# Optimization experiments

Measured on AMD Instinct MI355X. Metric: run time of the kernel, lower is better.

## Reference

```python
import math
import jax, jax.numpy as jnp
import numpy as np

E = 64   # embed_size (also per-head dim)
H = 8    # heads
B = 4
T = 2048


def setup_inputs() -> dict:
    key = jax.random.key(0)
    ks = jax.random.split(key, 8)
    s_in = 1.0 / math.sqrt(E)
    s_out = 1.0 / math.sqrt(H * E)
    return {
        "values": jax.random.normal(ks[0], (B, T, E), dtype=jnp.float32),
        "keys": jax.random.normal(ks[1], (B, T, E), dtype=jnp.float32),
        "queries": jax.random.normal(ks[2], (B, T, E), dtype=jnp.float32),
        # Linear(E, E*H, bias=False) weights, stored as [in, out] for x @ W
        "Wv": jax.random.uniform(ks[3], (E, E * H), jnp.float32, -s_in, s_in),
        "Wk": jax.random.uniform(ks[4], (E, E * H), jnp.float32, -s_in, s_in),
        "Wq": jax.random.uniform(ks[5], (E, E * H), jnp.float32, -s_in, s_in),
        # unifyheads: Linear(H*E, E)
        "Wu": jax.random.uniform(ks[6], (H * E, E), jnp.float32, -s_out, s_out),
        "bu": jax.random.uniform(ks[7], (E,), jnp.float32, -s_out, s_out),
    }


def reference(values, keys, queries, Wv, Wk, Wq, Wu, bu):
    b, t, e = keys.shape
    h = H
    v = (values @ Wv).reshape(b, t, h, e)   # bthe
    k = (keys @ Wk).reshape(b, t, h, e)
    q = (queries @ Wq).reshape(b, t, h, e)
    dot = jnp.einsum('bthe,bihe->bhti', q, k) / math.sqrt(e)  # [b,h,t,i]
    # NOTE: source applies softmax over dim=2 (the query axis t), faithfully kept
    attention = jax.nn.softmax(dot, axis=2)
    out = jnp.einsum('bhtd,bdhe->bthe', attention, v).reshape(b, t, h * e)
    return out @ Wu + bu
```

## Files before the change

### kernel.cpp

```cpp
#include <hip/hip_runtime.h>


typedef __attribute__((ext_vector_type(8))) __bf16 bf16x8;
typedef __attribute__((ext_vector_type(8))) unsigned short ushort8;
typedef __attribute__((ext_vector_type(4))) unsigned short ushort4v;
typedef __attribute__((ext_vector_type(4))) short short4v;
typedef __attribute__((ext_vector_type(4))) float f32x4;
typedef unsigned int uint32;

constexpr int B_ = 4;
constexpr int T_ = 2048;
constexpr int H_ = 8;
constexpr int E_ = 64;
constexpr int BH_ = B_ * H_;
constexpr int SZ_ = 8;
constexpr int NP_ = 2;
constexpr float QSCALE_ = 0.125f * 1.4426950408889634f;

__device__ inline uint32 f2bf1(float f) {
  uint32 u = __builtin_bit_cast(uint32, f);
  return (u + 0x7fffu + ((u >> 16) & 1u)) >> 16;
}
__device__ inline uint32 pk2(float a, float b) {
#if __has_builtin(__builtin_amdgcn_cvt_pk_bf16_f32)
  return __builtin_bit_cast(uint32, __builtin_amdgcn_cvt_pk_bf16_f32(a, b));
#else
  return f2bf1(a) | (f2bf1(b) << 16);
#endif
}
__device__ inline float bf2f(uint32 bits) {
  return __builtin_bit_cast(float, bits << 16);
}
__device__ inline bf16x8 ld8(const unsigned short* p) {
  return __builtin_bit_cast(bf16x8, *(const ushort8*)p);
}
__device__ inline short4v ld4(const unsigned short* p) {
  return __builtin_bit_cast(short4v, *(const ushort4v*)p);
}
#define MFMA16(a, b, c) __builtin_amdgcn_mfma_f32_16x16x32_bf16(a, b, c, 0, 0, 0)
#define EXP2(x) __builtin_amdgcn_exp2f(x)

__device__ inline f32x4 pv_mfma(short4v a, short4v b, f32x4 c) {
#if __has_builtin(__builtin_amdgcn_mfma_f32_16x16x16bf16_1k)
  return __builtin_amdgcn_mfma_f32_16x16x16bf16_1k(a, b, c, 0, 0, 0);
#else
  asm("v_mfma_f32_16x16x16_bf16 %0, %1, %2, %0" : "+v"(c) : "v"(a), "v"(b));
  return c;
#endif
}

__device__ inline void dma16(const unsigned short* g, unsigned short* l) {
  __builtin_amdgcn_global_load_lds(
      (const __attribute__((address_space(1))) void*)g,
      (__attribute__((address_space(3))) void*)l, 16, 0, 0);
}

__global__ __launch_bounds__(512) void proj_kernel(
    const float* __restrict__ Xq, const float* __restrict__ Xk,
    const float* __restrict__ Xv, const float* __restrict__ Wq,
    const float* __restrict__ Wk, const float* __restrict__ Wv,
    unsigned short* __restrict__ Yq, unsigned short* __restrict__ Yk,
    unsigned short* __restrict__ Yv) {
  constexpr int RT = 8;
  __shared__ float xs[RT][E_];
  const int z = blockIdx.y;
  const float* X = (z == 0) ? Xq : (z == 1) ? Xk : Xv;
  const float* W = (z == 0) ? Wq : (z == 1) ? Wk : Wv;
  unsigned short* Y = (z == 0) ? Yq : (z == 1) ? Yk : Yv;
  const float scale = (z == 0) ? QSCALE_ : 1.0f;
  const int row0 = blockIdx.x * RT;
  const int tid = threadIdx.x;
  {
    const int r = tid >> 6, c = tid & 63;
    xs[r][c] = X[(row0 + r) * E_ + c];
  }
  __syncthreads();
  const int j = tid;
  const int h = j >> 6, e = j & 63;
  float acc[RT];
#pragma unroll
  for (int r = 0; r < RT; ++r) acc[r] = 0.f;
  for (int c = 0; c < E_; ++c) {
    const float w = W[c * (H_ * E_) + j];
#pragma unroll
    for (int r = 0; r < RT; ++r) acc[r] += xs[r][c] * w;
  }
#pragma unroll
  for (int r = 0; r < RT; ++r) {
    const int row = row0 + r;
    const int b = row >> 11, t = row & (T_ - 1);
    Y[(((size_t)(b * H_ + h) * T_ + t) << 6) + e] =
        (unsigned short)f2bf1(acc[r] * scale);
  }
}

__global__ __launch_bounds__(256, 4) void stats_kernel(
    const unsigned short* __restrict__ K16, const unsigned short* __restrict__ Q16,
    float* __restrict__ s_part) {
  const int g = blockIdx.x;
  const int x = g & 7, s = g >> 3;
  const int bh = x + 8 * (s >> 6);
  const int rem = s & 63;
  const int zi = rem >> 3;
  const int dblk = rem & 7;
  const int tid = threadIdx.x;
  const int w = tid >> 6, lane = tid & 63;
  const int lm = lane & 15, lq = lane >> 4;
  const int d0 = dblk * 256 + w * 64;
  const int tz0 = zi * (T_ / SZ_);
  const unsigned short* Kp = K16 + (size_t)bh * T_ * E_;
  const unsigned short* Qp = Q16 + (size_t)bh * T_ * E_;

  bf16x8 kf[4][2];
#pragma unroll
  for (int dt = 0; dt < 4; ++dt) {
    kf[dt][0] = ld8(&Kp[(size_t)(d0 + dt * 16 + lm) * E_ + lq * 8]);
    kf[dt][1] = ld8(&Kp[(size_t)(d0 + dt * 16 + lm) * E_ + 32 + lq * 8]);
  }
  f32x4 sacc[4];
#pragma unroll
  for (int dt = 0; dt < 4; ++dt) sacc[dt] = (f32x4){0.f, 0.f, 0.f, 0.f};
  const f32x4 zero = {0.f, 0.f, 0.f, 0.f};

  for (int t0 = tz0; t0 < tz0 + 256; t0 += 16) {
    const bf16x8 ql = ld8(&Qp[(size_t)(t0 + lm) * E_ + lq * 8]);
    const bf16x8 qh = ld8(&Qp[(size_t)(t0 + lm) * E_ + 32 + lq * 8]);
#pragma unroll
    for (int dt = 0; dt < 4; ++dt) {
      f32x4 c = MFMA16(kf[dt][0], ql, zero);
      c = MFMA16(kf[dt][1], qh, c);
#pragma unroll
      for (int r = 0; r < 4; ++r) sacc[dt][r] += EXP2(c[r]);
    }
  }
#pragma unroll
  for (int m = 1; m < 16; m <<= 1) {
#pragma unroll
    for (int dt = 0; dt < 4; ++dt)
#pragma unroll
      for (int r = 0; r < 4; ++r)
        sacc[dt][r] += __shfl_xor(sacc[dt][r], m);
  }
  if (lm == 0) {
#pragma unroll
    for (int dt = 0; dt < 4; ++dt)
#pragma unroll
      for (int r = 0; r < 4; ++r)
        s_part[((size_t)zi * BH_ + bh) * T_ + d0 + dt * 16 + lq * 4 + r] =
            sacc[dt][r];
  }
}

__global__ __launch_bounds__(256) void scale_kernel(
    const unsigned short* __restrict__ V16, const float* __restrict__ s_part,
    unsigned short* __restrict__ Vt16) {
  __shared__ float ts[64][68];
  __shared__ float sinv_s[64];
  const int bh = blockIdx.y;
  const int d0 = blockIdx.x * 64;
  const unsigned short* Vp = V16 + (size_t)bh * T_ * E_;
  const int tid = threadIdx.x;
  if (tid < 64) {
    float s = 0.f;
#pragma unroll
    for (int z = 0; z < SZ_; ++z)
      s += s_part[((size_t)z * BH_ + bh) * T_ + d0 + tid];
    sinv_s[tid] = 1.0f / s;
  }
  __syncthreads();
  for (int idx = tid; idx < 64 * 8; idx += 256) {
    const int r = idx >> 3, c8 = idx & 7;
    const ushort8 v8 = *(const ushort8*)&Vp[(size_t)(d0 + r) * E_ + c8 * 8];
    const float is = sinv_s[r];
#pragma unroll
    for (int k = 0; k < 8; ++k) ts[r][c8 * 8 + k] = bf2f(v8[k]) * is;
  }
  __syncthreads();
  for (int idx = tid; idx < 64 * 16; idx += 256) {
    const int e = idx >> 4, d4 = idx & 15;
    uint2 o;
    o.x = pk2(ts[d4 * 4 + 0][e], ts[d4 * 4 + 1][e]);
    o.y = pk2(ts[d4 * 4 + 2][e], ts[d4 * 4 + 3][e]);
    *(uint2*)&Vt16[((size_t)bh * E_ + e) * T_ + d0 + d4 * 4] = o;
  }
}

__global__ __launch_bounds__(256, 4) void apply_kernel(
    const unsigned short* __restrict__ K16, const unsigned short* __restrict__ Q16,
    const unsigned short* __restrict__ Vt16, float* __restrict__ o_part) {
  __shared__ __align__(16) unsigned short K_s[2][32 * 64];
  __shared__ __align__(16) unsigned short V_s[2][64 * 32];
  const int g = blockIdx.x;
  const int xcd = g & 7, slot = g >> 3;
  const int bh = xcd + 8 * (slot >> 5);
  const int rem = slot & 31;
  const int np = rem >> 4;
  const int tblk = rem & 15;
  const int b = bh >> 3, h = bh & 7;
  const int tid = threadIdx.x;
  const int w = tid >> 6, lane = tid & 63;
  const int lm = lane & 15, lq = lane >> 4;
  const int t0 = tblk * 128 + w * 32;
  const int dbase = np * (T_ / NP_);
  constexpr int NC = (T_ / NP_) / 32;
  const unsigned short* Kp = K16 + (size_t)bh * T_ * E_;
  const unsigned short* Qp = Q16 + (size_t)bh * T_ * E_;
  const unsigned short* Vp = Vt16 + (size_t)bh * E_ * T_;

  const int kr = lane >> 3, kp = lane & 7, ks = kp ^ kr;
  const unsigned short* gK = Kp + (size_t)(w * 8 + kr) * E_ + ks * 8;
  const int ve = w * 16 + (lane >> 2), vseg = lane & 3;
  const unsigned short* gV = Vp + (size_t)ve * T_ + vseg * 8;
  unsigned short* lK0 = &K_s[0][w * 512];
  unsigned short* lK1 = &K_s[1][w * 512];
  unsigned short* lV0 = &V_s[0][w * 512];
  unsigned short* lV1 = &V_s[1][w * 512];

  bf16x8 qf[2][2];
#pragma unroll
  for (int tt = 0; tt < 2; ++tt) {
    qf[tt][0] = ld8(&Qp[(size_t)(t0 + tt * 16 + lm) * E_ + lq * 8]);
    qf[tt][1] = ld8(&Qp[(size_t)(t0 + tt * 16 + lm) * E_ + 32 + lq * 8]);
  }
  f32x4 acc[2][4];
#pragma unroll
  for (int tt = 0; tt < 2; ++tt)
#pragma unroll
    for (int ec = 0; ec < 4; ++ec) acc[tt][ec] = (f32x4){0.f, 0.f, 0.f, 0.f};
  const f32x4 zero = {0.f, 0.f, 0.f, 0.f};

  dma16(gK + (size_t)dbase * E_, lK0);
  dma16(gV + dbase, lV0);
  __syncthreads();

  for (int c = 0; c < NC; ++c) {
    const int cur = c & 1;
    if (c + 1 < NC) {
      const int dn = dbase + (c + 1) * 32;
      dma16(gK + (size_t)dn * E_, cur ? lK0 : lK1);
      dma16(gV + dn, cur ? lV0 : lV1);
    }
    const unsigned short* Kb = K_s[cur];
    const unsigned short* Vb = V_s[cur];
    bf16x8 kf[2][2];
#pragma unroll
    for (int half = 0; half < 2; ++half)
#pragma unroll
      for (int hi = 0; hi < 2; ++hi)
        kf[half][hi] =
            ld8(&Kb[(half * 16 + lm) * 64 + (((hi * 4 + lq) ^ (lm & 7)) * 8)]);
    short4v vf[4][2];
#pragma unroll
    for (int ec = 0; ec < 4; ++ec)
#pragma unroll
      for (int half = 0; half < 2; ++half)
        vf[ec][half] = ld4(&Vb[(ec * 16 + lm) * 32 + half * 16 + lq * 4]);

#pragma unroll
    for (int tt = 0; tt < 2; ++tt) {
      f32x4 c0 = MFMA16(kf[0][0], qf[tt][0], zero);
      c0 = MFMA16(kf[0][1], qf[tt][1], c0);
      f32x4 c1 = MFMA16(kf[1][0], qf[tt][0], zero);
      c1 = MFMA16(kf[1][1], qf[tt][1], c1);
      const uint32 b00 = pk2(EXP2(c0[0]), EXP2(c0[1]));
      const uint32 b01 = pk2(EXP2(c0[2]), EXP2(c0[3]));
      const uint32 b10 = pk2(EXP2(c1[0]), EXP2(c1[1]));
      const uint32 b11 = pk2(EXP2(c1[2]), EXP2(c1[3]));
      const short4v eB0 = __builtin_bit_cast(short4v, make_uint2(b00, b01));
      const short4v eB1 = __builtin_bit_cast(short4v, make_uint2(b10, b11));
#pragma unroll
      for (int ec = 0; ec < 4; ++ec) {
        acc[tt][ec] = pv_mfma(vf[ec][0], eB0, acc[tt][ec]);
        acc[tt][ec] = pv_mfma(vf[ec][1], eB1, acc[tt][ec]);
      }
    }
    __syncthreads();
  }

  float* op_base = o_part + (size_t)np * BH_ * T_ * E_;
#pragma unroll
  for (int tt = 0; tt < 2; ++tt) {
    const int t = t0 + tt * 16 + lm;
#pragma unroll
    for (int ec = 0; ec < 4; ++ec) {
      float* op = &op_base[((size_t)(b * T_ + t) * H_ + h) * E_ + ec * 16 + lq * 4];
      *(float4*)op = make_float4(acc[tt][ec][0], acc[tt][ec][1],
                                 acc[tt][ec][2], acc[tt][ec][3]);
    }
  }
}

__global__ __launch_bounds__(256) void unify_kernel(
    const float* __restrict__ o0, const float* __restrict__ o1,
    const float* __restrict__ Wu, const float* __restrict__ bu,
    float* __restrict__ out) {
  constexpr int RT = 16;
  __shared__ float xs[RT][H_ * E_];
  const int row0 = blockIdx.x * RT;
  const int tid = threadIdx.x;
  for (int idx = tid; idx < RT * 128; idx += 256) {
    const int r = idx >> 7, c4 = idx & 127;
    const float4 a = *(const float4*)&o0[(size_t)(row0 + r) * 512 + c4 * 4];
    const float4 bv = *(const float4*)&o1[(size_t)(row0 + r) * 512 + c4 * 4];
    xs[r][c4 * 4 + 0] = a.x + bv.x;
    xs[r][c4 * 4 + 1] = a.y + bv.y;
    xs[r][c4 * 4 + 2] = a.z + bv.z;
    xs[r][c4 * 4 + 3] = a.w + bv.w;
  }
  __syncthreads();
  const int j = tid & 63;
  const int rg = tid >> 6;
  float acc[4] = {0.f, 0.f, 0.f, 0.f};
  for (int c = 0; c < 512; ++c) {
    const float w = Wu[c * 64 + j];
#pragma unroll
    for (int r = 0; r < 4; ++r) acc[r] += xs[rg * 4 + r][c] * w;
  }
  const float bias = bu[j];
#pragma unroll
  for (int r = 0; r < 4; ++r)
    out[(size_t)(row0 + rg * 4 + r) * 64 + j] = acc[r] + bias;
}

extern "C" void kernel_launch(void* const* d_in, const int* in_sizes, int n_in,
                              void* d_out, int out_size, void* d_ws, size_t ws_size,
                              hipStream_t stream) {
  const float* values  = (const float*)d_in[0];
  const float* keys    = (const float*)d_in[1];
  const float* queries = (const float*)d_in[2];
  const float* Wv      = (const float*)d_in[3];
  const float* Wk      = (const float*)d_in[4];
  const float* Wq      = (const float*)d_in[5];
  const float* Wu      = (const float*)d_in[6];
  const float* bu      = (const float*)d_in[7];
  float* out = (float*)d_out;

  const size_t NQ = (size_t)BH_ * T_ * E_;
  unsigned short* q_bf  = (unsigned short*)d_ws;
  unsigned short* k_bf  = q_bf + NQ;
  unsigned short* v_bf  = k_bf + NQ;
  unsigned short* vt_bf = v_bf + NQ;
  float* o_ws   = (float*)(vt_bf + NQ);
  float* s_part = o_ws + (size_t)NP_ * NQ;

  proj_kernel<<<dim3(B_ * T_ / 8, 3), 512, 0, stream>>>(
      queries, keys, values, Wq, Wk, Wv, q_bf, k_bf, v_bf);
  stats_kernel<<<T_ / 256 * BH_ * SZ_, 256, 0, stream>>>(k_bf, q_bf, s_part);
  scale_kernel<<<dim3(T_ / 64, BH_), 256, 0, stream>>>(v_bf, s_part, vt_bf);
  apply_kernel<<<BH_ * (T_ / 128) * NP_, 256, 0, stream>>>(k_bf, q_bf, vt_bf, o_ws);
  unify_kernel<<<B_ * T_ / 16, 256, 0, stream>>>(o_ws, o_ws + NQ, Wu, bu, out);
}
```

Before: 289.6 us.

## Enlarge apply chunks with permuted V layout, stage Q in LDS for stats

The apply kernel now loads 64-key chunks of K and V per iteration instead of 32. The scale kernel writes V-transposed in a permuted order, so each lane fetches one 8-wide vector and splits it into the two 4-wide MFMA operands, replacing two narrower LDS reads. The stats kernel stages Q tiles through double-buffered LDS using async global-to-LDS loads instead of direct global loads. The projection kernel handles 16 rows per block to reuse weight loads. The changes raise LDS use per block, which may reduce occupancy.

```diff
diff --git a/kernel.cpp b/kernel.cpp
--- a/kernel.cpp
+++ b/kernel.cpp
@@ -2,8 +2,8 @@
 
 
 typedef __attribute__((ext_vector_type(8))) __bf16 bf16x8;
+typedef __attribute__((ext_vector_type(8))) short short8v;
 typedef __attribute__((ext_vector_type(8))) unsigned short ushort8;
-typedef __attribute__((ext_vector_type(4))) unsigned short ushort4v;
 typedef __attribute__((ext_vector_type(4))) short short4v;
 typedef __attribute__((ext_vector_type(4))) float f32x4;
 typedef unsigned int uint32;
@@ -34,8 +34,13 @@
 __device__ inline bf16x8 ld8(const unsigned short* p) {
   return __builtin_bit_cast(bf16x8, *(const ushort8*)p);
 }
-__device__ inline short4v ld4(const unsigned short* p) {
-  return __builtin_bit_cast(short4v, *(const ushort4v*)p);
+__device__ inline short4v lo4(bf16x8 v) {
+  short8v s = __builtin_bit_cast(short8v, v);
+  return __builtin_shufflevector(s, s, 0, 1, 2, 3);
+}
+__device__ inline short4v hi4(bf16x8 v) {
+  short8v s = __builtin_bit_cast(short8v, v);
+  return __builtin_shufflevector(s, s, 4, 5, 6, 7);
 }
 #define MFMA16(a, b, c) __builtin_amdgcn_mfma_f32_16x16x32_bf16(a, b, c, 0, 0, 0)
 #define EXP2(x) __builtin_amdgcn_exp2f(x)
@@ -61,7 +66,7 @@
     const float* __restrict__ Wk, const float* __restrict__ Wv,
     unsigned short* __restrict__ Yq, unsigned short* __restrict__ Yk,
     unsigned short* __restrict__ Yv) {
-  constexpr int RT = 8;
+  constexpr int RT = 16;
   __shared__ float xs[RT][E_];
   const int z = blockIdx.y;
   const float* X = (z == 0) ? Xq : (z == 1) ? Xk : Xv;
@@ -70,10 +75,9 @@
   const float scale = (z == 0) ? QSCALE_ : 1.0f;
   const int row0 = blockIdx.x * RT;
   const int tid = threadIdx.x;
-  {
-    const int r = tid >> 6, c = tid & 63;
-    xs[r][c] = X[(row0 + r) * E_ + c];
-  }
+#pragma unroll
+  for (int idx = tid; idx < RT * E_; idx += 512)
+    xs[idx >> 6][idx & 63] = X[(size_t)(row0 + (idx >> 6)) * E_ + (idx & 63)];
   __syncthreads();
   const int j = tid;
   const int h = j >> 6, e = j & 63;
@@ -97,6 +101,7 @@
 __global__ __launch_bounds__(256, 4) void stats_kernel(
     const unsigned short* __restrict__ K16, const unsigned short* __restrict__ Q16,
     float* __restrict__ s_part) {
+  __shared__ __align__(16) unsigned short Q_s[2][64 * 64];
   const int g = blockIdx.x;
   const int x = g & 7, s = g >> 3;
   const int bh = x + 8 * (s >> 6);
@@ -111,6 +116,12 @@
   const unsigned short* Kp = K16 + (size_t)bh * T_ * E_;
   const unsigned short* Qp = Q16 + (size_t)bh * T_ * E_;
 
+  const int kr = lane >> 3, kp = lane & 7;
+  const unsigned short* gQ =
+      Qp + (size_t)(tz0 + w * 16 + kr) * E_ + (kp ^ kr) * 8;
+  unsigned short* lQ0 = &Q_s[0][w * 1024];
+  unsigned short* lQ1 = &Q_s[1][w * 1024];
+
   bf16x8 kf[4][2];
 #pragma unroll
   for (int dt = 0; dt < 4; ++dt) {
@@ -122,16 +133,35 @@
   for (int dt = 0; dt < 4; ++dt) sacc[dt] = (f32x4){0.f, 0.f, 0.f, 0.f};
   const f32x4 zero = {0.f, 0.f, 0.f, 0.f};
 
-  for (int t0 = tz0; t0 < tz0 + 256; t0 += 16) {
-    const bf16x8 ql = ld8(&Qp[(size_t)(t0 + lm) * E_ + lq * 8]);
-    const bf16x8 qh = ld8(&Qp[(size_t)(t0 + lm) * E_ + 32 + lq * 8]);
-#pragma unroll
-    for (int dt = 0; dt < 4; ++dt) {
-      f32x4 c = MFMA16(kf[dt][0], ql, zero);
-      c = MFMA16(kf[dt][1], qh, c);
-#pragma unroll
-      for (int r = 0; r < 4; ++r) sacc[dt][r] += EXP2(c[r]);
-    }
+  dma16(gQ, lQ0);
+  dma16(gQ + 8 * E_, lQ0 + 512);
+  __syncthreads();
+
+  for (int c = 0; c < 4; ++c) {
+    const unsigned short* Qb = Q_s[c & 1];
+    bf16x8 qf[4][2];
+#pragma unroll
+    for (int tt = 0; tt < 4; ++tt)
+#pragma unroll
+      for (int half = 0; half < 2; ++half)
+        qf[tt][half] =
+            ld8(&Qb[(tt * 16 + lm) * 64 + (((half * 4 + lq) ^ (lm & 7)) * 8)]);
+    if (c < 3) {
+      const unsigned short* gn = gQ + (size_t)(c + 1) * 64 * E_;
+      unsigned short* ln = (c & 1) ? lQ0 : lQ1;
+      dma16(gn, ln);
+      dma16(gn + 8 * E_, ln + 512);
+    }
+#pragma unroll
+    for (int tt = 0; tt < 4; ++tt)
+#pragma unroll
+      for (int dt = 0; dt < 4; ++dt) {
+        f32x4 cc = MFMA16(kf[dt][0], qf[tt][0], zero);
+        cc = MFMA16(kf[dt][1], qf[tt][1], cc);
+#pragma unroll
+        for (int r = 0; r < 4; ++r) sacc[dt][r] += EXP2(cc[r]);
+      }
+    __syncthreads();
   }
 #pragma unroll
   for (int m = 1; m < 16; m <<= 1) {
@@ -177,19 +207,26 @@
   }
   __syncthreads();
   for (int idx = tid; idx < 64 * 16; idx += 256) {
-    const int e = idx >> 4, d4 = idx & 15;
-    uint2 o;
-    o.x = pk2(ts[d4 * 4 + 0][e], ts[d4 * 4 + 1][e]);
-    o.y = pk2(ts[d4 * 4 + 2][e], ts[d4 * 4 + 3][e]);
-    *(uint2*)&Vt16[((size_t)bh * E_ + e) * T_ + d0 + d4 * 4] = o;
+    const int e = idx >> 4, q = idx & 15;
+    float v[4];
+#pragma unroll
+    for (int j = 0; j < 4; ++j) {
+      const int pos = q * 4 + j;
+      const int c32 = pos >> 5, i = pos & 31;
+      const int lqp = i >> 3, u = i & 7;
+      const int dl = (u < 4) ? (lqp * 4 + u) : (16 + lqp * 4 + (u - 4));
+      v[j] = ts[c32 * 32 + dl][e];
+    }
+    uint2 o = make_uint2(pk2(v[0], v[1]), pk2(v[2], v[3]));
+    *(uint2*)&Vt16[((size_t)bh * E_ + e) * T_ + d0 + q * 4] = o;
   }
 }
 
 __global__ __launch_bounds__(256, 4) void apply_kernel(
     const unsigned short* __restrict__ K16, const unsigned short* __restrict__ Q16,
     const unsigned short* __restrict__ Vt16, float* __restrict__ o_part) {
-  __shared__ __align__(16) unsigned short K_s[2][32 * 64];
-  __shared__ __align__(16) unsigned short V_s[2][64 * 32];
+  __shared__ __align__(16) unsigned short K_s[2][64 * 64];
+  __shared__ __align__(16) unsigned short V_s[2][64 * 64];
   const int g = blockIdx.x;
   const int xcd = g & 7, slot = g >> 3;
   const int bh = xcd + 8 * (slot >> 5);
@@ -202,19 +239,18 @@
   const int lm = lane & 15, lq = lane >> 4;
   const int t0 = tblk * 128 + w * 32;
   const int dbase = np * (T_ / NP_);
-  constexpr int NC = (T_ / NP_) / 32;
+  constexpr int NC = (T_ / NP_) / 64;
   const unsigned short* Kp = K16 + (size_t)bh * T_ * E_;
   const unsigned short* Qp = Q16 + (size_t)bh * T_ * E_;
   const unsigned short* Vp = Vt16 + (size_t)bh * E_ * T_;
 
-  const int kr = lane >> 3, kp = lane & 7, ks = kp ^ kr;
-  const unsigned short* gK = Kp + (size_t)(w * 8 + kr) * E_ + ks * 8;
-  const int ve = w * 16 + (lane >> 2), vseg = lane & 3;
-  const unsigned short* gV = Vp + (size_t)ve * T_ + vseg * 8;
-  unsigned short* lK0 = &K_s[0][w * 512];
-  unsigned short* lK1 = &K_s[1][w * 512];
-  unsigned short* lV0 = &V_s[0][w * 512];
-  unsigned short* lV1 = &V_s[1][w * 512];
+  const int kr = lane >> 3, kp = lane & 7;
+  const unsigned short* gK = Kp + (size_t)(w * 16 + kr) * E_ + (kp ^ kr) * 8;
+  const unsigned short* gV = Vp + (size_t)(w * 16 + kr) * T_ + kp * 8;
+  unsigned short* lK0 = &K_s[0][w * 1024];
+  unsigned short* lK1 = &K_s[1][w * 1024];
+  unsigned short* lV0 = &V_s[0][w * 1024];
+  unsigned short* lV1 = &V_s[1][w * 1024];
 
   bf16x8 qf[2][2];
 #pragma unroll
@@ -230,48 +266,56 @@
   const f32x4 zero = {0.f, 0.f, 0.f, 0.f};
 
   dma16(gK + (size_t)dbase * E_, lK0);
+  dma16(gK + (size_t)dbase * E_ + 8 * E_, lK0 + 512);
   dma16(gV + dbase, lV0);
+  dma16(gV + dbase + 8 * T_, lV0 + 512);
   __syncthreads();
 
   for (int c = 0; c < NC; ++c) {
     const int cur = c & 1;
-    if (c + 1 < NC) {
-      const int dn = dbase + (c + 1) * 32;
-      dma16(gK + (size_t)dn * E_, cur ? lK0 : lK1);
-      dma16(gV + dn, cur ? lV0 : lV1);
-    }
     const unsigned short* Kb = K_s[cur];
     const unsigned short* Vb = V_s[cur];
-    bf16x8 kf[2][2];
-#pragma unroll
-    for (int half = 0; half < 2; ++half)
+    bf16x8 kf[4][2];
+#pragma unroll
+    for (int dd = 0; dd < 4; ++dd)
 #pragma unroll
       for (int hi = 0; hi < 2; ++hi)
-        kf[half][hi] =
-            ld8(&Kb[(half * 16 + lm) * 64 + (((hi * 4 + lq) ^ (lm & 7)) * 8)]);
-    short4v vf[4][2];
-#pragma unroll
-    for (int ec = 0; ec < 4; ++ec)
-#pragma unroll
-      for (int half = 0; half < 2; ++half)
-        vf[ec][half] = ld4(&Vb[(ec * 16 + lm) * 32 + half * 16 + lq * 4]);
-
-#pragma unroll
-    for (int tt = 0; tt < 2; ++tt) {
-      f32x4 c0 = MFMA16(kf[0][0], qf[tt][0], zero);
-      c0 = MFMA16(kf[0][1], qf[tt][1], c0);
-      f32x4 c1 = MFMA16(kf[1][0], qf[tt][0], zero);
-      c1 = MFMA16(kf[1][1], qf[tt][1], c1);
-      const uint32 b00 = pk2(EXP2(c0[0]), EXP2(c0[1]));
-      const uint32 b01 = pk2(EXP2(c0[2]), EXP2(c0[3]));
-      const uint32 b10 = pk2(EXP2(c1[0]), EXP2(c1[1]));
-      const uint32 b11 = pk2(EXP2(c1[2]), EXP2(c1[3]));
-      const short4v eB0 = __builtin_bit_cast(short4v, make_uint2(b00, b01));
-      const short4v eB1 = __builtin_bit_cast(short4v, make_uint2(b10, b11));
-#pragma unroll
-      for (int ec = 0; ec < 4; ++ec) {
-        acc[tt][ec] = pv_mfma(vf[ec][0], eB0, acc[tt][ec]);
-        acc[tt][ec] = pv_mfma(vf[ec][1], eB1, acc[tt][ec]);
+        kf[dd][hi] =
+            ld8(&Kb[(dd * 16 + lm) * 64 + (((hi * 4 + lq) ^ (lm & 7)) * 8)]);
+    bf16x8 vf[2][4];
+#pragma unroll
+    for (int h2 = 0; h2 < 2; ++h2)
+#pragma unroll
+      for (int ec = 0; ec < 4; ++ec)
+        vf[h2][ec] = ld8(&Vb[(ec * 16 + lm) * 64 + h2 * 32 + lq * 8]);
+    if (c + 1 < NC) {
+      const int dn = dbase + (c + 1) * 64;
+      unsigned short* nK = cur ? lK0 : lK1;
+      unsigned short* nV = cur ? lV0 : lV1;
+      dma16(gK + (size_t)dn * E_, nK);
+      dma16(gK + (size_t)dn * E_ + 8 * E_, nK + 512);
+      dma16(gV + dn, nV);
+      dma16(gV + dn + 8 * T_, nV + 512);
+    }
+#pragma unroll
+    for (int h2 = 0; h2 < 2; ++h2) {
+#pragma unroll
+      for (int tt = 0; tt < 2; ++tt) {
+        f32x4 c0 = MFMA16(kf[2 * h2][0], qf[tt][0], zero);
+        c0 = MFMA16(kf[2 * h2][1], qf[tt][1], c0);
+        f32x4 c1 = MFMA16(kf[2 * h2 + 1][0], qf[tt][0], zero);
+        c1 = MFMA16(kf[2 * h2 + 1][1], qf[tt][1], c1);
+        const uint32 b00 = pk2(EXP2(c0[0]), EXP2(c0[1]));
+        const uint32 b01 = pk2(EXP2(c0[2]), EXP2(c0[3]));
+        const uint32 b10 = pk2(EXP2(c1[0]), EXP2(c1[1]));
+        const uint32 b11 = pk2(EXP2(c1[2]), EXP2(c1[3]));
+        const short4v eB0 = __builtin_bit_cast(short4v, make_uint2(b00, b01));
+        const short4v eB1 = __builtin_bit_cast(short4v, make_uint2(b10, b11));
+#pragma unroll
+        for (int ec = 0; ec < 4; ++ec) {
+          acc[tt][ec] = pv_mfma(lo4(vf[h2][ec]), eB0, acc[tt][ec]);
+          acc[tt][ec] = pv_mfma(hi4(vf[h2][ec]), eB1, acc[tt][ec]);
+        }
       }
     }
     __syncthreads();
@@ -343,7 +387,7 @@
   float* o_ws   = (float*)(vt_bf + NQ);
   float* s_part = o_ws + (size_t)NP_ * NQ;
 
-  proj_kernel<<<dim3(B_ * T_ / 8, 3), 512, 0, stream>>>(
+  proj_kernel<<<dim3(B_ * T_ / 16, 3), 512, 0, stream>>>(
       queries, keys, values, Wq, Wk, Wv, q_bf, k_bf, v_bf);
   stats_kernel<<<T_ / 256 * BH_ * SZ_, 256, 0, stream>>>(k_bf, q_bf, s_part);
   scale_kernel<<<dim3(T_ / 64, BH_), 256, 0, stream>>>(v_bf, s_part, vt_bf);
```

After: 306.5 us. 1.06x slower.
